# Kernel optimization log

Measured on AMD Instinct MI355X. Metric: run time of the kernel, lower is better.

Reference implementation:

```python
import jax, jax.numpy as jnp
import numpy as np

INTER = 30
NPOOL = 33            # int(1000/30), matches AvgPool2d floor behavior
CA_SCALE = NPOOL ** 0.5
EMB, HEADS, DEPTH = 10, 5, 3


def _ln(x, g, b, eps=1e-5):
    m = jnp.mean(x, -1, keepdims=True)
    v = jnp.mean(jnp.square(x - m), -1, keepdims=True)
    return (x - m) * jax.lax.rsqrt(v + eps) * g + b


def _pool(x):
    # AvgPool2d(kernel=(1,INTER), stride=(1,INTER)) on last dim: [b,o,c,s] -> [b,o,c,NPOOL]
    b, o, c, s = x.shape
    return x[..., :NPOOL * INTER].reshape(b, o, c, NPOOL, INTER).mean(-1)


def _conv(x, w, strides):
    return jax.lax.conv_general_dilated(x, w, strides, 'VALID',
                                        dimension_numbers=('NCHW', 'OIHW', 'NCHW'))


def _channel_attention(x, qw, qb, qg, qbe, kw, kb, kg, kbe, pw, pb, pg, pbe):
    temp = jnp.swapaxes(x, -1, -2)                               # b o s c
    q = jnp.swapaxes(_ln(temp @ qw + qb, qg, qbe), -1, -2)       # b o c s
    k = jnp.swapaxes(_ln(temp @ kw + kb, kg, kbe), -1, -2)
    att = jnp.einsum('bocs,boms->bocm', _pool(q), _pool(k)) / CA_SCALE
    score = jax.nn.softmax(att, axis=-1)
    out = jnp.einsum('bocs,bocm->bocs', x, score)                # m summed out, as in torch einsum
    out = _ln(jnp.swapaxes(out, -1, -2) @ pw + pb, pg, pbe)
    return jnp.swapaxes(out, -1, -2)


def _mha(x, qw, qb, kw, kb, vw, vb, ow, ob):
    b, n, e = x.shape
    d = e // HEADS
    q = (x @ qw + qb).reshape(b, n, HEADS, d).transpose(0, 2, 1, 3)
    k = (x @ kw + kb).reshape(b, n, HEADS, d).transpose(0, 2, 1, 3)
    v = (x @ vw + vb).reshape(b, n, HEADS, d).transpose(0, 2, 1, 3)
    energy = jnp.einsum('bhqd,bhkd->bhqk', q, k)
    att = jax.nn.softmax(energy / (e ** 0.5), axis=-1)
    out = jnp.einsum('bhqk,bhkd->bhqd', att, v)
    return out.transpose(0, 2, 1, 3).reshape(b, n, e) @ ow + ob


def setup_inputs():
    key = jax.random.key(0)
    ks = jax.random.split(key, 16)
    g = lambda i, sh, s=0.1: jax.random.normal(ks[i], sh, jnp.float32) * s
    z = lambda sh: jnp.zeros(sh, jnp.float32)
    o = lambda sh: jnp.ones(sh, jnp.float32)
    return dict(
        x=jax.random.normal(ks[0], (512, 1, 1000, 22), jnp.float32),
        change_w=g(1, (22, 16)), change_b=z((16,)),
        ca_q_w=g(2, (16, 16)), ca_q_b=z((16,)), ca_q_g=o((16,)), ca_q_be=z((16,)),
        ca_k_w=g(3, (16, 16)), ca_k_b=z((16,)), ca_k_g=o((16,)), ca_k_be=z((16,)),
        ca_p_w=g(4, (16, 16)), ca_p_b=z((16,)), ca_p_g=o((16,)), ca_p_be=z((16,)),
        conv1_w=g(5, (2, 1, 1, 51)), conv1_b=z((2,)),
        bn_g=o((2,)), bn_b=z((2,)), bn_mean=z((2,)), bn_var=o((2,)),
        conv2_w=g(6, (10, 2, 16, 5)), conv2_b=z((10,)),
        tf_ln1_g=o((3, 10)), tf_ln1_b=z((3, 10)),
        tf_q_w=g(7, (3, 10, 10)), tf_q_b=z((3, 10)),
        tf_k_w=g(8, (3, 10, 10)), tf_k_b=z((3, 10)),
        tf_v_w=g(9, (3, 10, 10)), tf_v_b=z((3, 10)),
        tf_o_w=g(10, (3, 10, 10)), tf_o_b=z((3, 10)),
        tf_ln2_g=o((3, 10)), tf_ln2_b=z((3, 10)),
        tf_ff1_w=g(11, (3, 10, 40)), tf_ff1_b=z((3, 40)),
        tf_ff2_w=g(12, (3, 40, 10)), tf_ff2_b=z((3, 10)),
    )


def reference(x, change_w, change_b,
              ca_q_w, ca_q_b, ca_q_g, ca_q_be,
              ca_k_w, ca_k_b, ca_k_g, ca_k_be,
              ca_p_w, ca_p_b, ca_p_g, ca_p_be,
              conv1_w, conv1_b, bn_g, bn_b, bn_mean, bn_var,
              conv2_w, conv2_b,
              tf_ln1_g, tf_ln1_b, tf_q_w, tf_q_b, tf_k_w, tf_k_b,
              tf_v_w, tf_v_b, tf_o_w, tf_o_b, tf_ln2_g, tf_ln2_b,
              tf_ff1_w, tf_ff1_b, tf_ff2_w, tf_ff2_b):
    h = x @ change_w + change_b                  # [b,1,1000,16]
    h = jnp.swapaxes(h, -1, -2)                  # [b,1,16,1000]
    for _ in range(4):
        h = _channel_attention(h, ca_q_w, ca_q_b, ca_q_g, ca_q_be,
                               ca_k_w, ca_k_b, ca_k_g, ca_k_be,
                               ca_p_w, ca_p_b, ca_p_g, ca_p_be) + h
    c = _conv(h, conv1_w, (1, 1)) + conv1_b[None, :, None, None]     # [b,2,16,950]
    bshape = lambda v: v[None, :, None, None]
    c = (c - bshape(bn_mean)) * bshape(jax.lax.rsqrt(bn_var + 1e-5)) * bshape(bn_g) + bshape(bn_b)
    c = jnp.where(c > 0, c, 0.2 * c)             # LeakyReLU(0.2)
    c = _conv(c, conv2_w, (1, 5)) + conv2_b[None, :, None, None]     # [b,10,1,190]
    b_, e_, hh, ww = c.shape
    t = c.reshape(b_, e_, hh * ww).transpose(0, 2, 1)                # [b,190,10]
    for i in range(DEPTH):
        y = _ln(t, tf_ln1_g[i], tf_ln1_b[i])
        t = t + _mha(y, tf_q_w[i], tf_q_b[i], tf_k_w[i], tf_k_b[i],
                     tf_v_w[i], tf_v_b[i], tf_o_w[i], tf_o_b[i])
        y = _ln(t, tf_ln2_g[i], tf_ln2_b[i])
        t = t + (jax.nn.gelu(y @ tf_ff1_w[i] + tf_ff1_b[i], approximate=False) @ tf_ff2_w[i] + tf_ff2_b[i])
    return t
```

## Files before the change

kernel.cpp:

```cpp
#include <hip/hip_runtime.h>

using ushort_t = unsigned short;

__device__ __forceinline__ float u2f(ushort_t u){
    union{unsigned int i; float f;} x; x.i = ((unsigned int)u) << 16; return x.f;
}
__device__ __forceinline__ ushort_t f2u(float f){
    union{float fl; unsigned int i;} x; x.fl = f;
    unsigned int r = x.i + 0x7FFFu + ((x.i >> 16) & 1u);
    return (ushort_t)(r >> 16);
}

__device__ __forceinline__ void ln10(const float* in, float* out,
                                     const float* __restrict__ g,
                                     const float* __restrict__ b){
    float m = 0.f;
#pragma unroll
    for (int c = 0; c < 10; ++c) m += in[c];
    m *= 0.1f;
    float v = 0.f;
#pragma unroll
    for (int c = 0; c < 10; ++c){ float d = in[c] - m; v += d*d; }
    v *= 0.1f;
    float inv = rsqrtf(v + 1e-5f);
#pragma unroll
    for (int c = 0; c < 10; ++c) out[c] = (in[c] - m) * inv * g[c] + b[c];
}

__global__ __launch_bounds__(256)
void k_embed(const float* __restrict__ X,
             const float* __restrict__ CW, const float* __restrict__ CB,
             const float* __restrict__ PW, const float* __restrict__ PB,
             const float* __restrict__ PG, const float* __restrict__ PBE,
             ushort_t* __restrict__ Hws)
{
    const int idx = blockIdx.x * 256 + threadIdx.x;
    const int b = idx / 1000, s = idx - b * 1000;

    const float2* xu = (const float2*)(X + (size_t)idx * 22);
    float xv[22];
#pragma unroll
    for (int j = 0; j < 11; ++j){
        float2 u = xu[j];
        xv[2*j] = u.x; xv[2*j+1] = u.y;
    }
    float v[16];
#pragma unroll
    for (int c = 0; c < 16; ++c){
        float a = CB[c];
#pragma unroll
        for (int j = 0; j < 22; ++j) a += xv[j] * CW[j*16 + c];
        v[c] = a;
    }
#pragma unroll
    for (int it = 0; it < 4; ++it){
        float u[16]; float m = 0.f;
#pragma unroll
        for (int c = 0; c < 16; ++c){
            float a = PB[c];
#pragma unroll
            for (int j = 0; j < 16; ++j) a += v[j] * PW[j*16 + c];
            u[c] = a; m += a;
        }
        m *= (1.f/16.f);
        float var = 0.f;
#pragma unroll
        for (int c = 0; c < 16; ++c){ float d = u[c] - m; var += d*d; }
        var *= (1.f/16.f);
        float inv = rsqrtf(var + 1e-5f);
#pragma unroll
        for (int c = 0; c < 16; ++c) v[c] += (u[c] - m) * inv * PG[c] + PBE[c];
    }
#pragma unroll
    for (int c = 0; c < 16; ++c)
        Hws[b*16000 + c*1000 + s] = f2u(v[c]);
}

__global__ __launch_bounds__(256)
void k_conv(const ushort_t* __restrict__ Hws,
            const float* __restrict__ W1, const float* __restrict__ B1,
            const float* __restrict__ BNG, const float* __restrict__ BNB,
            const float* __restrict__ BNM, const float* __restrict__ BNV,
            const float* __restrict__ W2, const float* __restrict__ B2,
            float* __restrict__ Tws)
{
    __shared__ __align__(16) float sH[16000];

    const int tid = threadIdx.x;
    const int b   = blockIdx.x;

    for (int i = tid; i < 16000; i += 256) sH[i] = u2f(Hws[b*16000 + i]);

    float sc[2], sh[2];
#pragma unroll
    for (int i = 0; i < 2; ++i){
        float s0 = BNG[i] * rsqrtf(BNV[i] + 1e-5f);
        sc[i] = s0;
        sh[i] = BNB[i] + (B1[i] - BNM[i]) * s0;
    }
    __syncthreads();

    if (tid < 190){
        const int w = tid;
        float acc[10];
#pragma unroll
        for (int o = 0; o < 10; ++o) acc[o] = B2[o];
        for (int kh = 0; kh < 16; ++kh){
            float hh[55];
#pragma unroll
            for (int j = 0; j < 55; ++j) hh[j] = sH[kh*1000 + 5*w + j];
            float val[2][5];
#pragma unroll
            for (int i = 0; i < 2; ++i){
#pragma unroll
                for (int kw = 0; kw < 5; ++kw){
                    float s = 0.f;
#pragma unroll
                    for (int k = 0; k < 51; ++k) s += hh[kw + k] * W1[i*51 + k];
                    s = s * sc[i] + sh[i];
                    val[i][kw] = s > 0.f ? s : 0.2f * s;
                }
            }
#pragma unroll
            for (int o = 0; o < 10; ++o){
                float s = acc[o];
#pragma unroll
                for (int i = 0; i < 2; ++i)
#pragma unroll
                    for (int kw = 0; kw < 5; ++kw)
                        s += val[i][kw] * W2[((o*2 + i)*16 + kh)*5 + kw];
                acc[o] = s;
            }
        }
#pragma unroll
        for (int o = 0; o < 10; ++o) Tws[(size_t)b*1900 + w*10 + o] = acc[o];
    }
}

__global__ __launch_bounds__(256)
void k_tf(const float* __restrict__ Tws,
          const float* __restrict__ LN1G, const float* __restrict__ LN1B,
          const float* __restrict__ QW, const float* __restrict__ QBv,
          const float* __restrict__ KW, const float* __restrict__ KBv,
          const float* __restrict__ VW, const float* __restrict__ VBv,
          const float* __restrict__ OW, const float* __restrict__ OBv,
          const float* __restrict__ LN2G, const float* __restrict__ LN2B,
          const float* __restrict__ F1W, const float* __restrict__ F1B,
          const float* __restrict__ F2W, const float* __restrict__ F2B,
          float* __restrict__ OUT)
{
    __shared__ __align__(16) float T [190*11];
    __shared__ __align__(16) float QB[190*12];
    __shared__ __align__(16) float KB[190*12];
    __shared__ __align__(16) float VB[190*12];
    __shared__ __align__(16) float AT[190*12];

    const int tid = threadIdx.x;
    const int b   = blockIdx.x;

    for (int i = tid; i < 1900; i += 256){
        int r = i / 10, c = i - r*10;
        T[r*11 + c] = Tws[(size_t)b*1900 + i];
    }
    __syncthreads();

    const float SCALE = 0.31622776601683794f;
    const bool act = (tid < 190);
#pragma unroll 1
    for (int L = 0; L < 3; ++L){
        const float* ln1g = LN1G + L*10; const float* ln1b = LN1B + L*10;
        const float* qw = QW + L*100;    const float* qb = QBv + L*10;
        const float* kw = KW + L*100;    const float* kb = KBv + L*10;
        const float* vw = VW + L*100;    const float* vb = VBv + L*10;
        const float* ow = OW + L*100;    const float* ob = OBv + L*10;
        const float* ln2g = LN2G + L*10; const float* ln2b = LN2B + L*10;
        const float* f1w = F1W + L*400;  const float* f1b = F1B + L*40;
        const float* f2w = F2W + L*400;  const float* f2b = F2B + L*10;

        if (act){
            float tv[10], y[10];
#pragma unroll
            for (int c = 0; c < 10; ++c) tv[c] = T[tid*11 + c];
            ln10(tv, y, ln1g, ln1b);
#pragma unroll
            for (int c = 0; c < 10; ++c){
                float aq = qb[c], ak = kb[c], av = vb[c];
#pragma unroll
                for (int j = 0; j < 10; ++j){
                    aq += y[j] * qw[j*10 + c];
                    ak += y[j] * kw[j*10 + c];
                    av += y[j] * vw[j*10 + c];
                }
                QB[tid*12 + c] = aq;
                KB[tid*12 + c] = ak;
                VB[tid*12 + c] = av;
            }
        }
        __syncthreads();

        if (tid < 240){
            const int h5 = tid / 48;
            const int qg = tid - h5*48;
            const int q0 = qg * 4;
            float qx[4], qy[4];
#pragma unroll
            for (int i = 0; i < 4; ++i){
                int qi = q0 + i;
                if (qi < 190){
                    qx[i] = QB[qi*12 + 2*h5]     * SCALE;
                    qy[i] = QB[qi*12 + 2*h5 + 1] * SCALE;
                } else { qx[i] = 0.f; qy[i] = 0.f; }
            }
            float l[4] = {0,0,0,0}, a0[4] = {0,0,0,0}, a1[4] = {0,0,0,0};
#pragma unroll 2
            for (int kk = 0; kk < 190; ++kk){
                float2 kv = *(const float2*)&KB[kk*12 + 2*h5];
                float2 vv = *(const float2*)&VB[kk*12 + 2*h5];
#pragma unroll
                for (int i = 0; i < 4; ++i){
                    float p = __expf(qx[i]*kv.x + qy[i]*kv.y);
                    l[i] += p; a0[i] += p*vv.x; a1[i] += p*vv.y;
                }
            }
#pragma unroll
            for (int i = 0; i < 4; ++i){
                int qi = q0 + i;
                if (qi < 190){
                    float rl = 1.f / l[i];
                    AT[qi*12 + 2*h5]     = a0[i] * rl;
                    AT[qi*12 + 2*h5 + 1] = a1[i] * rl;
                }
            }
        }
        __syncthreads();

        if (act){
            float tv[10], at[10];
#pragma unroll
            for (int c = 0; c < 10; ++c){ tv[c] = T[tid*11 + c]; at[c] = AT[tid*12 + c]; }
#pragma unroll
            for (int c = 0; c < 10; ++c){
                float a = ob[c];
#pragma unroll
                for (int j = 0; j < 10; ++j) a += at[j] * ow[j*10 + c];
                tv[c] += a;
            }
            float y2[10];
            ln10(tv, y2, ln2g, ln2b);
            float g40[40];
#pragma unroll
            for (int j = 0; j < 40; ++j){
                float a = f1b[j];
#pragma unroll
                for (int c = 0; c < 10; ++c) a += y2[c] * f1w[c*40 + j];
                g40[j] = 0.5f * a * (1.f + erff(a * 0.70710678118654752f));
            }
#pragma unroll
            for (int c = 0; c < 10; ++c){
                float a = f2b[c];
#pragma unroll
                for (int j = 0; j < 40; ++j) a += g40[j] * f2w[j*10 + c];
                tv[c] += a;
            }
#pragma unroll
            for (int c = 0; c < 10; ++c) T[tid*11 + c] = tv[c];
        }
        __syncthreads();
    }

    if (act){
#pragma unroll
        for (int c = 0; c < 10; ++c)
            OUT[(size_t)b*1900 + tid*10 + c] = T[tid*11 + c];
    }
}

extern "C" void kernel_launch(void* const* d_in, const int* in_sizes, int n_in,
                              void* d_out, int out_size, void* d_ws, size_t ws_size,
                              hipStream_t stream)
{
    (void)ws_size; (void)n_in; (void)out_size;
    const int B = in_sizes[0] / 22000;
    auto in = [&](int i){ return (const float*)d_in[i]; };
    ushort_t* Hws = (ushort_t*)d_ws;
    float*    Tws = (float*)((char*)d_ws + (size_t)B*16000*2);

    k_embed<<<(B*1000 + 255)/256, 256, 0, stream>>>(
        in(0), in(1), in(2), in(11), in(12), in(13), in(14), Hws);

    k_conv<<<B, 256, 0, stream>>>(
        Hws, in(15), in(16), in(17), in(18), in(19), in(20), in(21), in(22), Tws);

    k_tf<<<B, 256, 0, stream>>>(
        Tws,
        in(23), in(24), in(25), in(26), in(27), in(28), in(29), in(30),
        in(31), in(32), in(33), in(34), in(35), in(36), in(37), in(38),
        (float*)d_out);
}
```

Measured before the change: 485.5 us.

## Fuse conv and transformer kernels, restructure conv stage, stage weights in LDS

Merges the conv and transformer kernels into one per-batch kernel, so the intermediate T tensor stays in shared memory instead of going through global memory. The first conv stage is reorganised: 6080 work items spread across all 256 threads each compute a 5-wide window and write bf16 results to LDS, where before 190 threads recomputed everything. The embed kernel now stages its weights in LDS, processes two rows per thread with float4 weight reads, and uses a fixed 1000-block grid. The transformer weights are also copied into LDS, and the FFN is fused so the 40-wide hidden array is not kept live. Risks are the hardcoded batch of 512 in the embed grid and row stride, heavy LDS use (about 67 KB) limiting occupancy, and an extra bf16 rounding of the intermediate conv output.

```diff
diff --git a/kernel.cpp b/kernel.cpp
--- a/kernel.cpp
+++ b/kernel.cpp
@@ -9,22 +9,6 @@
     union{float fl; unsigned int i;} x; x.fl = f;
     unsigned int r = x.i + 0x7FFFu + ((x.i >> 16) & 1u);
     return (ushort_t)(r >> 16);
-}
-
-__device__ __forceinline__ void ln10(const float* in, float* out,
-                                     const float* __restrict__ g,
-                                     const float* __restrict__ b){
-    float m = 0.f;
-#pragma unroll
-    for (int c = 0; c < 10; ++c) m += in[c];
-    m *= 0.1f;
-    float v = 0.f;
-#pragma unroll
-    for (int c = 0; c < 10; ++c){ float d = in[c] - m; v += d*d; }
-    v *= 0.1f;
-    float inv = rsqrtf(v + 1e-5f);
-#pragma unroll
-    for (int c = 0; c < 10; ++c) out[c] = (in[c] - m) * inv * g[c] + b[c];
 }
 
 __global__ __launch_bounds__(256)
@@ -34,133 +18,210 @@
              const float* __restrict__ PG, const float* __restrict__ PBE,
              ushort_t* __restrict__ Hws)
 {
-    const int idx = blockIdx.x * 256 + threadIdx.x;
-    const int b = idx / 1000, s = idx - b * 1000;
-
-    const float2* xu = (const float2*)(X + (size_t)idx * 22);
-    float xv[22];
-#pragma unroll
-    for (int j = 0; j < 11; ++j){
-        float2 u = xu[j];
-        xv[2*j] = u.x; xv[2*j+1] = u.y;
-    }
-    float v[16];
-#pragma unroll
-    for (int c = 0; c < 16; ++c){
-        float a = CB[c];
-#pragma unroll
-        for (int j = 0; j < 22; ++j) a += xv[j] * CW[j*16 + c];
-        v[c] = a;
-    }
+    __shared__ __align__(16) float sW[672];
+    {
+        const int t = threadIdx.x;
+        for (int i = t; i < 352; i += 256) sW[i] = CW[i];
+        if (t < 256) { if (t < 16){ sW[352+t] = CB[t]; sW[624+t] = PB[t];
+                                    sW[640+t] = PG[t]; sW[656+t] = PBE[t]; } }
+        for (int i = t; i < 256; i += 256) sW[368+i] = PW[i];
+    }
+    __syncthreads();
+    const float4* sW4 = (const float4*)sW;
+
+    const int g = blockIdx.x * 256 + threadIdx.x;
+
+    float xv[2][22];
+#pragma unroll
+    for (int r = 0; r < 2; ++r){
+        const float* xp = X + (size_t)(g + r*256000) * 22;
+#pragma unroll
+        for (int j = 0; j < 22; ++j) xv[r][j] = xp[j];
+    }
+
+    float v[2][16];
+#pragma unroll
+    for (int cg = 0; cg < 4; ++cg){
+        float acc[2][4];
+#pragma unroll
+        for (int q = 0; q < 4; ++q){ float b0 = sW[352 + cg*4 + q]; acc[0][q] = b0; acc[1][q] = b0; }
+#pragma unroll
+        for (int j = 0; j < 22; ++j){
+            float4 w = sW4[j*4 + cg];
+#pragma unroll
+            for (int r = 0; r < 2; ++r){
+                acc[r][0] += xv[r][j]*w.x; acc[r][1] += xv[r][j]*w.y;
+                acc[r][2] += xv[r][j]*w.z; acc[r][3] += xv[r][j]*w.w;
+            }
+        }
+#pragma unroll
+        for (int r = 0; r < 2; ++r)
+#pragma unroll
+        for (int q = 0; q < 4; ++q) v[r][cg*4+q] = acc[r][q];
+    }
+
 #pragma unroll
     for (int it = 0; it < 4; ++it){
-        float u[16]; float m = 0.f;
-#pragma unroll
-        for (int c = 0; c < 16; ++c){
-            float a = PB[c];
-#pragma unroll
-            for (int j = 0; j < 16; ++j) a += v[j] * PW[j*16 + c];
-            u[c] = a; m += a;
-        }
-        m *= (1.f/16.f);
-        float var = 0.f;
-#pragma unroll
-        for (int c = 0; c < 16; ++c){ float d = u[c] - m; var += d*d; }
-        var *= (1.f/16.f);
-        float inv = rsqrtf(var + 1e-5f);
-#pragma unroll
-        for (int c = 0; c < 16; ++c) v[c] += (u[c] - m) * inv * PG[c] + PBE[c];
-    }
-#pragma unroll
-    for (int c = 0; c < 16; ++c)
-        Hws[b*16000 + c*1000 + s] = f2u(v[c]);
+        float u[2][16];
+#pragma unroll
+        for (int cg = 0; cg < 4; ++cg){
+            float acc[2][4];
+#pragma unroll
+            for (int q = 0; q < 4; ++q){ float b0 = sW[624 + cg*4 + q]; acc[0][q] = b0; acc[1][q] = b0; }
+#pragma unroll
+            for (int j = 0; j < 16; ++j){
+                float4 w = sW4[92 + j*4 + cg];
+#pragma unroll
+                for (int r = 0; r < 2; ++r){
+                    acc[r][0] += v[r][j]*w.x; acc[r][1] += v[r][j]*w.y;
+                    acc[r][2] += v[r][j]*w.z; acc[r][3] += v[r][j]*w.w;
+                }
+            }
+#pragma unroll
+            for (int r = 0; r < 2; ++r)
+#pragma unroll
+            for (int q = 0; q < 4; ++q) u[r][cg*4+q] = acc[r][q];
+        }
+#pragma unroll
+        for (int r = 0; r < 2; ++r){
+            float m = 0.f;
+#pragma unroll
+            for (int c = 0; c < 16; ++c) m += u[r][c];
+            m *= (1.f/16.f);
+            float var = 0.f;
+#pragma unroll
+            for (int c = 0; c < 16; ++c){ float d = u[r][c] - m; var += d*d; }
+            var *= (1.f/16.f);
+            float inv = rsqrtf(var + 1e-5f);
+#pragma unroll
+            for (int c = 0; c < 16; ++c) v[r][c] += (u[r][c] - m) * inv * sW[640+c] + sW[656+c];
+        }
+    }
+
+#pragma unroll
+    for (int r = 0; r < 2; ++r){
+        const int row = g + r*256000;
+        const int b = row / 1000, s = row - b*1000;
+        ushort_t* hp = Hws + b*16000 + s;
+#pragma unroll
+        for (int c = 0; c < 16; ++c) hp[c*1000] = f2u(v[r][c]);
+    }
 }
 
 __global__ __launch_bounds__(256)
-void k_conv(const ushort_t* __restrict__ Hws,
+void k_main(const ushort_t* __restrict__ Hws,
             const float* __restrict__ W1, const float* __restrict__ B1,
             const float* __restrict__ BNG, const float* __restrict__ BNB,
             const float* __restrict__ BNM, const float* __restrict__ BNV,
             const float* __restrict__ W2, const float* __restrict__ B2,
-            float* __restrict__ Tws)
+            const float* __restrict__ LN1G, const float* __restrict__ LN1B,
+            const float* __restrict__ QW, const float* __restrict__ QBv,
+            const float* __restrict__ KW, const float* __restrict__ KBv,
+            const float* __restrict__ VW, const float* __restrict__ VBv,
+            const float* __restrict__ OW, const float* __restrict__ OBv,
+            const float* __restrict__ LN2G, const float* __restrict__ LN2B,
+            const float* __restrict__ F1W, const float* __restrict__ F1B,
+            const float* __restrict__ F2W, const float* __restrict__ F2B,
+            float* __restrict__ OUT)
 {
-    __shared__ __align__(16) float sH[16000];
-
+    __shared__ __align__(16) char sMem[67760];
     const int tid = threadIdx.x;
     const int b   = blockIdx.x;
 
-    for (int i = tid; i < 16000; i += 256) sH[i] = u2f(Hws[b*16000 + i]);
-
-    float sc[2], sh[2];
-#pragma unroll
-    for (int i = 0; i < 2; ++i){
-        float s0 = BNG[i] * rsqrtf(BNV[i] + 1e-5f);
-        sc[i] = s0;
-        sh[i] = BNB[i] + (B1[i] - BNM[i]) * s0;
-    }
-    __syncthreads();
-
+    ushort_t* C1  = (ushort_t*)sMem;
+    float*    W1f = (float*)(sMem + 60928);
+    float*    BNf = (float*)(sMem + 61344);
+    float*    W2f = (float*)(sMem + 61360);
+
+    for (int i = tid; i < 102;  i += 256) W1f[i] = W1[i];
+    for (int i = tid; i < 1600; i += 256) W2f[i] = W2[i];
+    if (tid < 2){
+        float s0 = BNG[tid] * rsqrtf(BNV[tid] + 1e-5f);
+        BNf[tid]     = s0;
+        BNf[2 + tid] = BNB[tid] + (B1[tid] - BNM[tid]) * s0;
+    }
+    __syncthreads();
+
+#pragma unroll 1
+    for (int k = 0; k < 24; ++k){
+        int gp = tid + 256*k;
+        if (gp < 6080){
+            const int ik = gp / 190;
+            const int u_ = gp - ik*190;
+            const int i  = ik >> 4;
+            const int kh = ik & 15;
+            const int w0 = u_ * 5;
+            const ushort_t* hp = Hws + b*16000 + kh*1000 + w0;
+            const float* w1p = W1f + i*51;
+            const float sc = BNf[i], sh = BNf[2+i];
+            float win[55];
+#pragma unroll
+            for (int t = 0; t < 55; ++t) win[t] = u2f(hp[t]);
+            float acc[5];
+#pragma unroll
+            for (int q = 0; q < 5; ++q) acc[q] = 0.f;
+#pragma unroll
+            for (int t = 0; t < 51; ++t){
+                float wk = w1p[t];
+#pragma unroll
+                for (int q = 0; q < 5; ++q) acc[q] += win[t+q] * wk;
+            }
+#pragma unroll
+            for (int q = 0; q < 5; ++q){
+                float s = acc[q]*sc + sh;
+                s = s > 0.f ? s : 0.2f*s;
+                C1[ik*952 + w0 + q] = f2u(s);
+            }
+        }
+    }
+    __syncthreads();
+
+    float acc10[10];
     if (tid < 190){
-        const int w = tid;
-        float acc[10];
-#pragma unroll
-        for (int o = 0; o < 10; ++o) acc[o] = B2[o];
+        const ushort_t* c1p = C1 + tid*5;
+#pragma unroll
+        for (int o = 0; o < 10; ++o) acc10[o] = B2[o];
+#pragma unroll
         for (int kh = 0; kh < 16; ++kh){
-            float hh[55];
-#pragma unroll
-            for (int j = 0; j < 55; ++j) hh[j] = sH[kh*1000 + 5*w + j];
-            float val[2][5];
-#pragma unroll
-            for (int i = 0; i < 2; ++i){
-#pragma unroll
-                for (int kw = 0; kw < 5; ++kw){
-                    float s = 0.f;
-#pragma unroll
-                    for (int k = 0; k < 51; ++k) s += hh[kw + k] * W1[i*51 + k];
-                    s = s * sc[i] + sh[i];
-                    val[i][kw] = s > 0.f ? s : 0.2f * s;
-                }
-            }
-#pragma unroll
-            for (int o = 0; o < 10; ++o){
-                float s = acc[o];
-#pragma unroll
-                for (int i = 0; i < 2; ++i)
-#pragma unroll
-                    for (int kw = 0; kw < 5; ++kw)
-                        s += val[i][kw] * W2[((o*2 + i)*16 + kh)*5 + kw];
-                acc[o] = s;
-            }
-        }
-#pragma unroll
-        for (int o = 0; o < 10; ++o) Tws[(size_t)b*1900 + w*10 + o] = acc[o];
-    }
-}
-
-__global__ __launch_bounds__(256)
-void k_tf(const float* __restrict__ Tws,
-          const float* __restrict__ LN1G, const float* __restrict__ LN1B,
-          const float* __restrict__ QW, const float* __restrict__ QBv,
-          const float* __restrict__ KW, const float* __restrict__ KBv,
-          const float* __restrict__ VW, const float* __restrict__ VBv,
-          const float* __restrict__ OW, const float* __restrict__ OBv,
-          const float* __restrict__ LN2G, const float* __restrict__ LN2B,
-          const float* __restrict__ F1W, const float* __restrict__ F1B,
-          const float* __restrict__ F2W, const float* __restrict__ F2B,
-          float* __restrict__ OUT)
-{
-    __shared__ __align__(16) float T [190*11];
-    __shared__ __align__(16) float QB[190*12];
-    __shared__ __align__(16) float KB[190*12];
-    __shared__ __align__(16) float VB[190*12];
-    __shared__ __align__(16) float AT[190*12];
-
-    const int tid = threadIdx.x;
-    const int b   = blockIdx.x;
-
-    for (int i = tid; i < 1900; i += 256){
-        int r = i / 10, c = i - r*10;
-        T[r*11 + c] = Tws[(size_t)b*1900 + i];
+#pragma unroll
+            for (int kw = 0; kw < 5; ++kw){
+                float v0 = u2f(c1p[ kh*952       + kw]);
+                float v1 = u2f(c1p[(16+kh)*952   + kw]);
+#pragma unroll
+                for (int o = 0; o < 10; ++o)
+                    acc10[o] += v0 * W2f[((o*2    )*16 + kh)*5 + kw]
+                              + v1 * W2f[((o*2 + 1)*16 + kh)*5 + kw];
+            }
+        }
+    }
+    __syncthreads();
+
+    float* TW = (float*)sMem;
+    float* T  = (float*)(sMem + 15960);
+    float* QB = (float*)(sMem + 24320);
+    float* KB = (float*)(sMem + 33440);
+    float* VB = (float*)(sMem + 42560);
+    float* AT = (float*)(sMem + 51680);
+
+    {
+        auto cl3 = [&](int off, const float* src, int n){
+            for (int i = tid; i < 3*n; i += 256){
+                int L = i / n, j = i - L*n;
+                TW[L*1330 + off + j] = src[i];
+            }
+        };
+        cl3(   0, LN1G,  10);  cl3(  10, LN1B,  10);
+        cl3(  20, QW,   100);  cl3( 120, QBv,   10);
+        cl3( 130, KW,   100);  cl3( 230, KBv,   10);
+        cl3( 240, VW,   100);  cl3( 340, VBv,   10);
+        cl3( 350, OW,   100);  cl3( 450, OBv,   10);
+        cl3( 460, LN2G,  10);  cl3( 470, LN2B,  10);
+        cl3( 480, F1W,  400);  cl3( 880, F1B,   40);
+        cl3( 920, F2W,  400);  cl3(1320, F2B,   10);
+    }
+    if (tid < 190){
+#pragma unroll
+        for (int o = 0; o < 10; ++o) T[tid*11 + o] = acc10[o];
     }
     __syncthreads();
 
@@ -168,28 +229,31 @@
     const bool act = (tid < 190);
 #pragma unroll 1
     for (int L = 0; L < 3; ++L){
-        const float* ln1g = LN1G + L*10; const float* ln1b = LN1B + L*10;
-        const float* qw = QW + L*100;    const float* qb = QBv + L*10;
-        const float* kw = KW + L*100;    const float* kb = KBv + L*10;
-        const float* vw = VW + L*100;    const float* vb = VBv + L*10;
-        const float* ow = OW + L*100;    const float* ob = OBv + L*10;
-        const float* ln2g = LN2G + L*10; const float* ln2b = LN2B + L*10;
-        const float* f1w = F1W + L*400;  const float* f1b = F1B + L*40;
-        const float* f2w = F2W + L*400;  const float* f2b = F2B + L*10;
+        const float* W = TW + L*1330;
 
         if (act){
             float tv[10], y[10];
 #pragma unroll
             for (int c = 0; c < 10; ++c) tv[c] = T[tid*11 + c];
-            ln10(tv, y, ln1g, ln1b);
+            float m = 0.f;
+#pragma unroll
+            for (int c = 0; c < 10; ++c) m += tv[c];
+            m *= 0.1f;
+            float var = 0.f;
+#pragma unroll
+            for (int c = 0; c < 10; ++c){ float d = tv[c]-m; var += d*d; }
+            var *= 0.1f;
+            float inv = rsqrtf(var + 1e-5f);
+#pragma unroll
+            for (int c = 0; c < 10; ++c) y[c] = (tv[c]-m)*inv*W[0+c] + W[10+c];
 #pragma unroll
             for (int c = 0; c < 10; ++c){
-                float aq = qb[c], ak = kb[c], av = vb[c];
+                float aq = W[120+c], ak = W[230+c], av = W[340+c];
 #pragma unroll
                 for (int j = 0; j < 10; ++j){
-                    aq += y[j] * qw[j*10 + c];
-                    ak += y[j] * kw[j*10 + c];
-                    av += y[j] * vw[j*10 + c];
+                    aq += y[j] * W[ 20 + j*10 + c];
+                    ak += y[j] * W[130 + j*10 + c];
+                    av += y[j] * W[240 + j*10 + c];
                 }
                 QB[tid*12 + c] = aq;
                 KB[tid*12 + c] = ak;
@@ -212,10 +276,12 @@
                 } else { qx[i] = 0.f; qy[i] = 0.f; }
             }
             float l[4] = {0,0,0,0}, a0[4] = {0,0,0,0}, a1[4] = {0,0,0,0};
+            const float* kp = KB + 2*h5;
+            const float* vp = VB + 2*h5;
 #pragma unroll 2
             for (int kk = 0; kk < 190; ++kk){
-                float2 kv = *(const float2*)&KB[kk*12 + 2*h5];
-                float2 vv = *(const float2*)&VB[kk*12 + 2*h5];
+                float2 kv = *(const float2*)(kp + kk*12);
+                float2 vv = *(const float2*)(vp + kk*12);
 #pragma unroll
                 for (int i = 0; i < 4; ++i){
                     float p = __expf(qx[i]*kv.x + qy[i]*kv.y);
@@ -240,30 +306,37 @@
             for (int c = 0; c < 10; ++c){ tv[c] = T[tid*11 + c]; at[c] = AT[tid*12 + c]; }
 #pragma unroll
             for (int c = 0; c < 10; ++c){
-                float a = ob[c];
-#pragma unroll
-                for (int j = 0; j < 10; ++j) a += at[j] * ow[j*10 + c];
+                float a = W[450+c];
+#pragma unroll
+                for (int j = 0; j < 10; ++j) a += at[j] * W[350 + j*10 + c];
                 tv[c] += a;
             }
+            float m = 0.f;
+#pragma unroll
+            for (int c = 0; c < 10; ++c) m += tv[c];
+            m *= 0.1f;
+            float var = 0.f;
+#pragma unroll
+            for (int c = 0; c < 10; ++c){ float d = tv[c]-m; var += d*d; }
+            var *= 0.1f;
+            float inv = rsqrtf(var + 1e-5f);
             float y2[10];
-            ln10(tv, y2, ln2g, ln2b);
-            float g40[40];
+#pragma unroll
+            for (int c = 0; c < 10; ++c) y2[c] = (tv[c]-m)*inv*W[460+c] + W[470+c];
+            float d10[10];
+#pragma unroll
+            for (int c = 0; c < 10; ++c) d10[c] = W[1320+c];
 #pragma unroll
             for (int j = 0; j < 40; ++j){
-                float a = f1b[j];
-#pragma unroll
-                for (int c = 0; c < 10; ++c) a += y2[c] * f1w[c*40 + j];
-                g40[j] = 0.5f * a * (1.f + erff(a * 0.70710678118654752f));
-            }
-#pragma unroll
-            for (int c = 0; c < 10; ++c){
-                float a = f2b[c];
-#pragma unroll
-                for (int j = 0; j < 40; ++j) a += g40[j] * f2w[j*10 + c];
-                tv[c] += a;
-            }
-#pragma unroll
-            for (int c = 0; c < 10; ++c) T[tid*11 + c] = tv[c];
+                float a = W[880+j];
+#pragma unroll
+                for (int c = 0; c < 10; ++c) a += y2[c] * W[480 + c*40 + j];
+                float gj = 0.5f * a * (1.f + erff(a * 0.70710678118654752f));
+#pragma unroll
+                for (int c = 0; c < 10; ++c) d10[c] += gj * W[920 + j*10 + c];
+            }
+#pragma unroll
+            for (int c = 0; c < 10; ++c) T[tid*11 + c] = tv[c] + d10[c];
         }
         __syncthreads();
     }
@@ -283,16 +356,13 @@
     const int B = in_sizes[0] / 22000;
     auto in = [&](int i){ return (const float*)d_in[i]; };
     ushort_t* Hws = (ushort_t*)d_ws;
-    float*    Tws = (float*)((char*)d_ws + (size_t)B*16000*2);
-
-    k_embed<<<(B*1000 + 255)/256, 256, 0, stream>>>(
+
+    k_embed<<<1000, 256, 0, stream>>>(
         in(0), in(1), in(2), in(11), in(12), in(13), in(14), Hws);
 
-    k_conv<<<B, 256, 0, stream>>>(
-        Hws, in(15), in(16), in(17), in(18), in(19), in(20), in(21), in(22), Tws);
-
-    k_tf<<<B, 256, 0, stream>>>(
-        Tws,
+    k_main<<<B, 256, 0, stream>>>(
+        Hws,
+        in(15), in(16), in(17), in(18), in(19), in(20), in(21), in(22),
         in(23), in(24), in(25), in(26), in(27), in(28), in(29), in(30),
         in(31), in(32), in(33), in(34), in(35), in(36), in(37), in(38),
         (float*)d_out);
```

Result: slower. 496.9 us (+2.4%).

## Macro-unroll all kernels into scalar registers and store conv input as bf16 in LDS

Applied to the files above, without the earlier changes.

Replaces the array-based loops in the embed, conv and transformer kernels with macro-expanded scalar variables so that everything stays in registers. The conv kernel now keeps its shared tile as bf16 (halving LDS to 32KB, which could allow more resident blocks), copies it with 32-bit loads, and converts values at each tap. The FFN computes the GELU hidden units in a loop and accumulates the second matmul on the fly instead of holding a 40-element array. The risks are heavier code size, register pressure, and extra per-tap conversion work in the conv inner loop.

```diff
diff --git a/kernel.cpp b/kernel.cpp
--- a/kernel.cpp
+++ b/kernel.cpp
@@ -1,6 +1,6 @@
 #include <hip/hip_runtime.h>
 
-using ushort_t = unsigned short;
+typedef unsigned short ushort_t;
 
 __device__ __forceinline__ float u2f(ushort_t u){
     union{unsigned int i; float f;} x; x.i = ((unsigned int)u) << 16; return x.f;
@@ -11,21 +11,10 @@
     return (ushort_t)(r >> 16);
 }
 
-__device__ __forceinline__ void ln10(const float* in, float* out,
-                                     const float* __restrict__ g,
-                                     const float* __restrict__ b){
-    float m = 0.f;
-#pragma unroll
-    for (int c = 0; c < 10; ++c) m += in[c];
-    m *= 0.1f;
-    float v = 0.f;
-#pragma unroll
-    for (int c = 0; c < 10; ++c){ float d = in[c] - m; v += d*d; }
-    v *= 0.1f;
-    float inv = rsqrtf(v + 1e-5f);
-#pragma unroll
-    for (int c = 0; c < 10; ++c) out[c] = (in[c] - m) * inv * g[c] + b[c];
-}
+#define REP10(M) M(0)M(1)M(2)M(3)M(4)M(5)M(6)M(7)M(8)M(9)
+#define REP16(M) M(0)M(1)M(2)M(3)M(4)M(5)M(6)M(7)M(8)M(9)M(10)M(11)M(12)M(13)M(14)M(15)
+#define REP22(M) REP16(M) M(16)M(17)M(18)M(19)M(20)M(21)
+#define REP55(M) M(0)M(1)M(2)M(3)M(4)M(5)M(6)M(7)M(8)M(9)M(10)M(11)M(12)M(13)M(14)M(15)M(16)M(17)M(18)M(19)M(20)M(21)M(22)M(23)M(24)M(25)M(26)M(27)M(28)M(29)M(30)M(31)M(32)M(33)M(34)M(35)M(36)M(37)M(38)M(39)M(40)M(41)M(42)M(43)M(44)M(45)M(46)M(47)M(48)M(49)M(50)M(51)M(52)M(53)M(54)
 
 __global__ __launch_bounds__(256)
 void k_embed(const float* __restrict__ X,
@@ -36,44 +25,42 @@
 {
     const int idx = blockIdx.x * 256 + threadIdx.x;
     const int b = idx / 1000, s = idx - b * 1000;
-
-    const float2* xu = (const float2*)(X + (size_t)idx * 22);
-    float xv[22];
-#pragma unroll
-    for (int j = 0; j < 11; ++j){
-        float2 u = xu[j];
-        xv[2*j] = u.x; xv[2*j+1] = u.y;
-    }
-    float v[16];
-#pragma unroll
-    for (int c = 0; c < 16; ++c){
-        float a = CB[c];
-#pragma unroll
-        for (int j = 0; j < 22; ++j) a += xv[j] * CW[j*16 + c];
-        v[c] = a;
-    }
-#pragma unroll
-    for (int it = 0; it < 4; ++it){
-        float u[16]; float m = 0.f;
-#pragma unroll
-        for (int c = 0; c < 16; ++c){
-            float a = PB[c];
-#pragma unroll
-            for (int j = 0; j < 16; ++j) a += v[j] * PW[j*16 + c];
-            u[c] = a; m += a;
-        }
-        m *= (1.f/16.f);
-        float var = 0.f;
-#pragma unroll
-        for (int c = 0; c < 16; ++c){ float d = u[c] - m; var += d*d; }
-        var *= (1.f/16.f);
-        float inv = rsqrtf(var + 1e-5f);
-#pragma unroll
-        for (int c = 0; c < 16; ++c) v[c] += (u[c] - m) * inv * PG[c] + PBE[c];
-    }
-#pragma unroll
-    for (int c = 0; c < 16; ++c)
-        Hws[b*16000 + c*1000 + s] = f2u(v[c]);
+    const float* xp = X + (size_t)idx * 22;
+
+#define E_DX(j) float x##j = xp[j];
+    REP22(E_DX)
+#define E_DV(c) float v##c = CB[c];
+    REP16(E_DV)
+#define E_CH(j) { const float xx = x##j; const float* w = CW + (j)*16; \
+    v0+=xx*w[0]; v1+=xx*w[1]; v2+=xx*w[2]; v3+=xx*w[3]; \
+    v4+=xx*w[4]; v5+=xx*w[5]; v6+=xx*w[6]; v7+=xx*w[7]; \
+    v8+=xx*w[8]; v9+=xx*w[9]; v10+=xx*w[10]; v11+=xx*w[11]; \
+    v12+=xx*w[12]; v13+=xx*w[13]; v14+=xx*w[14]; v15+=xx*w[15]; }
+    REP22(E_CH)
+
+#define E_DU(c) float u##c = PB[c];
+#define E_PJ(j) { const float vv = v##j; const float* w = PW + (j)*16; \
+    u0+=vv*w[0]; u1+=vv*w[1]; u2+=vv*w[2]; u3+=vv*w[3]; \
+    u4+=vv*w[4]; u5+=vv*w[5]; u6+=vv*w[6]; u7+=vv*w[7]; \
+    u8+=vv*w[8]; u9+=vv*w[9]; u10+=vv*w[10]; u11+=vv*w[11]; \
+    u12+=vv*w[12]; u13+=vv*w[13]; u14+=vv*w[14]; u15+=vv*w[15]; }
+#define E_DS(c) const float d##c = u##c - m;
+#define E_UP(c) v##c += d##c * inv * PG[c] + PBE[c];
+#define E_LNIT { \
+    REP16(E_DU) REP16(E_PJ) \
+    float m = (((u0+u1)+(u2+u3))+((u4+u5)+(u6+u7)))+(((u8+u9)+(u10+u11))+((u12+u13)+(u14+u15))); \
+    m *= 0.0625f; \
+    REP16(E_DS) \
+    float var = (((d0*d0+d1*d1)+(d2*d2+d3*d3))+((d4*d4+d5*d5)+(d6*d6+d7*d7)))+(((d8*d8+d9*d9)+(d10*d10+d11*d11))+((d12*d12+d13*d13)+(d14*d14+d15*d15))); \
+    var *= 0.0625f; \
+    float inv = rsqrtf(var + 1e-5f); \
+    REP16(E_UP) }
+
+    E_LNIT E_LNIT E_LNIT E_LNIT
+
+    ushort_t* hp = Hws + b*16000 + s;
+#define E_ST(c) hp[(c)*1000] = f2u(v##c);
+    REP16(E_ST)
 }
 
 __global__ __launch_bounds__(256)
@@ -84,56 +71,49 @@
             const float* __restrict__ W2, const float* __restrict__ B2,
             float* __restrict__ Tws)
 {
-    __shared__ __align__(16) float sH[16000];
-
-    const int tid = threadIdx.x;
-    const int b   = blockIdx.x;
-
-    for (int i = tid; i < 16000; i += 256) sH[i] = u2f(Hws[b*16000 + i]);
-
-    float sc[2], sh[2];
-#pragma unroll
-    for (int i = 0; i < 2; ++i){
-        float s0 = BNG[i] * rsqrtf(BNV[i] + 1e-5f);
-        sc[i] = s0;
-        sh[i] = BNB[i] + (B1[i] - BNM[i]) * s0;
-    }
+    __shared__ ushort_t sH[16000];
+    const int tid = threadIdx.x, b = blockIdx.x;
+
+    {
+        const unsigned int* src = (const unsigned int*)(Hws + b*16000);
+        unsigned int* dst = (unsigned int*)sH;
+        for (int i = tid; i < 8000; i += 256) dst[i] = src[i];
+    }
+    const float sc0 = BNG[0]*rsqrtf(BNV[0]+1e-5f);
+    const float sc1 = BNG[1]*rsqrtf(BNV[1]+1e-5f);
+    const float sh0 = BNB[0] + (B1[0]-BNM[0])*sc0;
+    const float sh1 = BNB[1] + (B1[1]-BNM[1])*sc1;
     __syncthreads();
 
     if (tid < 190){
-        const int w = tid;
-        float acc[10];
-#pragma unroll
-        for (int o = 0; o < 10; ++o) acc[o] = B2[o];
+        const int w5 = tid*5;
+#define C_DT(o) float t##o = B2[o];
+        REP10(C_DT)
+        const float* w1a = W1;
+        const float* w1b = W1 + 51;
         for (int kh = 0; kh < 16; ++kh){
-            float hh[55];
-#pragma unroll
-            for (int j = 0; j < 55; ++j) hh[j] = sH[kh*1000 + 5*w + j];
-            float val[2][5];
-#pragma unroll
-            for (int i = 0; i < 2; ++i){
-#pragma unroll
-                for (int kw = 0; kw < 5; ++kw){
-                    float s = 0.f;
-#pragma unroll
-                    for (int k = 0; k < 51; ++k) s += hh[kw + k] * W1[i*51 + k];
-                    s = s * sc[i] + sh[i];
-                    val[i][kw] = s > 0.f ? s : 0.2f * s;
-                }
-            }
-#pragma unroll
-            for (int o = 0; o < 10; ++o){
-                float s = acc[o];
-#pragma unroll
-                for (int i = 0; i < 2; ++i)
-#pragma unroll
-                    for (int kw = 0; kw < 5; ++kw)
-                        s += val[i][kw] * W2[((o*2 + i)*16 + kh)*5 + kw];
-                acc[o] = s;
-            }
-        }
-#pragma unroll
-        for (int o = 0; o < 10; ++o) Tws[(size_t)b*1900 + w*10 + o] = acc[o];
+            const ushort_t* hp = sH + kh*1000 + w5;
+            float a0=0.f,a1=0.f,a2=0.f,a3=0.f,a4=0.f;
+            float b0_=0.f,b1_=0.f,b2_=0.f,b3_=0.f,b4_=0.f;
+#define C_TAP(e) { const float cur = u2f(hp[e]); \
+            if ((e) < 51)              { a0+=cur*w1a[(e)];   b0_+=cur*w1b[(e)];   } \
+            if ((e) >= 1 && (e) < 52)  { a1+=cur*w1a[(e)-1]; b1_+=cur*w1b[(e)-1]; } \
+            if ((e) >= 2 && (e) < 53)  { a2+=cur*w1a[(e)-2]; b2_+=cur*w1b[(e)-2]; } \
+            if ((e) >= 3 && (e) < 54)  { a3+=cur*w1a[(e)-3]; b3_+=cur*w1b[(e)-3]; } \
+            if ((e) >= 4)              { a4+=cur*w1a[(e)-4]; b4_+=cur*w1b[(e)-4]; } }
+            REP55(C_TAP)
+#define C_LR(q) { a##q = a##q*sc0 + sh0; a##q = a##q > 0.f ? a##q : 0.2f*a##q; \
+                  b##q##_ = b##q##_*sc1 + sh1; b##q##_ = b##q##_ > 0.f ? b##q##_ : 0.2f*b##q##_; }
+            C_LR(0) C_LR(1) C_LR(2) C_LR(3) C_LR(4)
+#define C_C2(o) { const float* wa = W2 + (((o)*2  )*16 + kh)*5; \
+                  const float* wb = W2 + (((o)*2+1)*16 + kh)*5; \
+        t##o += a0*wa[0]+a1*wa[1]+a2*wa[2]+a3*wa[3]+a4*wa[4] \
+              + b0_*wb[0]+b1_*wb[1]+b2_*wb[2]+b3_*wb[3]+b4_*wb[4]; }
+            REP10(C_C2)
+        }
+        float* op = Tws + (size_t)b*1900 + tid*10;
+#define C_ST(o) op[o] = t##o;
+        REP10(C_ST)
     }
 }
 
@@ -155,11 +135,9 @@
     __shared__ __align__(16) float VB[190*12];
     __shared__ __align__(16) float AT[190*12];
 
-    const int tid = threadIdx.x;
-    const int b   = blockIdx.x;
-
+    const int tid = threadIdx.x, b = blockIdx.x;
     for (int i = tid; i < 1900; i += 256){
-        int r = i / 10, c = i - r*10;
+        int r = i/10, c = i - r*10;
         T[r*11 + c] = Tws[(size_t)b*1900 + i];
     }
     __syncthreads();
@@ -178,23 +156,29 @@
         const float* f2w = F2W + L*400;  const float* f2b = F2B + L*10;
 
         if (act){
-            float tv[10], y[10];
-#pragma unroll
-            for (int c = 0; c < 10; ++c) tv[c] = T[tid*11 + c];
-            ln10(tv, y, ln1g, ln1b);
-#pragma unroll
-            for (int c = 0; c < 10; ++c){
-                float aq = qb[c], ak = kb[c], av = vb[c];
-#pragma unroll
-                for (int j = 0; j < 10; ++j){
-                    aq += y[j] * qw[j*10 + c];
-                    ak += y[j] * kw[j*10 + c];
-                    av += y[j] * vw[j*10 + c];
-                }
-                QB[tid*12 + c] = aq;
-                KB[tid*12 + c] = ak;
-                VB[tid*12 + c] = av;
-            }
+#define T_TV(c) float tv##c = T[tid*11 + c];
+            REP10(T_TV)
+            float m = (((tv0+tv1)+(tv2+tv3))+((tv4+tv5)+(tv6+tv7)))+(tv8+tv9);
+            m *= 0.1f;
+#define T_D1(c) const float e1##c = tv##c - m;
+            REP10(T_D1)
+            float var = (((e10*e10+e11*e11)+(e12*e12+e13*e13))+((e14*e14+e15*e15)+(e16*e16+e17*e17)))+(e18*e18+e19*e19);
+            var *= 0.1f;
+            float inv = rsqrtf(var + 1e-5f);
+#define T_Y(c) const float y##c = e1##c*inv*ln1g[c] + ln1b[c];
+            REP10(T_Y)
+#define T_PQ(c) { float aq = qb[c] + y0*qw[c] + y1*qw[10+c] + y2*qw[20+c] + y3*qw[30+c] + y4*qw[40+c] \
+                           + y5*qw[50+c] + y6*qw[60+c] + y7*qw[70+c] + y8*qw[80+c] + y9*qw[90+c]; \
+                  QB[tid*12 + c] = aq; }
+            REP10(T_PQ)
+#define T_PK(c) { float ak = kb[c] + y0*kw[c] + y1*kw[10+c] + y2*kw[20+c] + y3*kw[30+c] + y4*kw[40+c] \
+                           + y5*kw[50+c] + y6*kw[60+c] + y7*kw[70+c] + y8*kw[80+c] + y9*kw[90+c]; \
+                  KB[tid*12 + c] = ak; }
+            REP10(T_PK)
+#define T_PV(c) { float av = vb[c] + y0*vw[c] + y1*vw[10+c] + y2*vw[20+c] + y3*vw[30+c] + y4*vw[40+c] \
+                           + y5*vw[50+c] + y6*vw[60+c] + y7*vw[70+c] + y8*vw[80+c] + y9*vw[90+c]; \
+                  VB[tid*12 + c] = av; }
+            REP10(T_PV)
         }
         __syncthreads();
 
@@ -202,76 +186,70 @@
             const int h5 = tid / 48;
             const int qg = tid - h5*48;
             const int q0 = qg * 4;
-            float qx[4], qy[4];
-#pragma unroll
-            for (int i = 0; i < 4; ++i){
-                int qi = q0 + i;
-                if (qi < 190){
-                    qx[i] = QB[qi*12 + 2*h5]     * SCALE;
-                    qy[i] = QB[qi*12 + 2*h5 + 1] * SCALE;
-                } else { qx[i] = 0.f; qy[i] = 0.f; }
+#define T_LQ(i) float qx##i, qy##i; { const int qi = q0 + i; \
+            if (qi < 190){ qx##i = QB[qi*12 + 2*h5]*SCALE; qy##i = QB[qi*12 + 2*h5 + 1]*SCALE; } \
+            else { qx##i = 0.f; qy##i = 0.f; } }
+            T_LQ(0) T_LQ(1) T_LQ(2) T_LQ(3)
+            float l0=0.f,l1=0.f,l2=0.f,l3=0.f;
+            float p00=0.f,p01=0.f,p10=0.f,p11=0.f,p20=0.f,p21=0.f,p30=0.f,p31=0.f;
+            const float* kp = KB + 2*h5;
+            const float* vp = VB + 2*h5;
+            for (int kk = 0; kk < 190; ++kk){
+                const float2 kv = *(const float2*)(kp + kk*12);
+                const float2 vv = *(const float2*)(vp + kk*12);
+                const float e0 = __expf(qx0*kv.x + qy0*kv.y);
+                const float e1 = __expf(qx1*kv.x + qy1*kv.y);
+                const float e2 = __expf(qx2*kv.x + qy2*kv.y);
+                const float e3 = __expf(qx3*kv.x + qy3*kv.y);
+                l0 += e0; p00 += e0*vv.x; p01 += e0*vv.y;
+                l1 += e1; p10 += e1*vv.x; p11 += e1*vv.y;
+                l2 += e2; p20 += e2*vv.x; p21 += e2*vv.y;
+                l3 += e3; p30 += e3*vv.x; p31 += e3*vv.y;
             }
-            float l[4] = {0,0,0,0}, a0[4] = {0,0,0,0}, a1[4] = {0,0,0,0};
-#pragma unroll 2
-            for (int kk = 0; kk < 190; ++kk){
-                float2 kv = *(const float2*)&KB[kk*12 + 2*h5];
-                float2 vv = *(const float2*)&VB[kk*12 + 2*h5];
-#pragma unroll
-                for (int i = 0; i < 4; ++i){
-                    float p = __expf(qx[i]*kv.x + qy[i]*kv.y);
-                    l[i] += p; a0[i] += p*vv.x; a1[i] += p*vv.y;
-                }
+#define T_SA(i) { const int qi = q0 + i; if (qi < 190){ const float rl = 1.f/l##i; \
+                  AT[qi*12 + 2*h5] = p##i##0*rl; AT[qi*12 + 2*h5 + 1] = p##i##1*rl; } }
+            T_SA(0) T_SA(1) T_SA(2) T_SA(3)
+        }
+        __syncthreads();
+
+        if (act){
+#define T_TV2(c) float w##c = T[tid*11 + c];
+            REP10(T_TV2)
+#define T_AT(c) const float at##c = AT[tid*12 + c];
+            REP10(T_AT)
+#define T_OP(c) w##c += ob[c] + at0*ow[c] + at1*ow[10+c] + at2*ow[20+c] + at3*ow[30+c] + at4*ow[40+c] \
+                       + at5*ow[50+c] + at6*ow[60+c] + at7*ow[70+c] + at8*ow[80+c] + at9*ow[90+c];
+            REP10(T_OP)
+            float m2 = (((w0+w1)+(w2+w3))+((w4+w5)+(w6+w7)))+(w8+w9);
+            m2 *= 0.1f;
+#define T_D2(c) const float e2##c = w##c - m2;
+            REP10(T_D2)
+            float var2 = (((e20*e20+e21*e21)+(e22*e22+e23*e23))+((e24*e24+e25*e25)+(e26*e26+e27*e27)))+(e28*e28+e29*e29);
+            var2 *= 0.1f;
+            float inv2 = rsqrtf(var2 + 1e-5f);
+#define T_Z(c) const float z##c = e2##c*inv2*ln2g[c] + ln2b[c];
+            REP10(T_Z)
+#define T_DD(c) float dd##c = f2b[c];
+            REP10(T_DD)
+#pragma unroll 4
+            for (int j = 0; j < 40; ++j){
+                float aj = f1b[j] + z0*f1w[j] + z1*f1w[40+j] + z2*f1w[80+j] + z3*f1w[120+j] + z4*f1w[160+j]
+                         + z5*f1w[200+j] + z6*f1w[240+j] + z7*f1w[280+j] + z8*f1w[320+j] + z9*f1w[360+j];
+                const float gj = 0.5f * aj * (1.f + erff(aj * 0.70710678118654752f));
+                const float* w2p = f2w + j*10;
+                dd0 += gj*w2p[0]; dd1 += gj*w2p[1]; dd2 += gj*w2p[2]; dd3 += gj*w2p[3]; dd4 += gj*w2p[4];
+                dd5 += gj*w2p[5]; dd6 += gj*w2p[6]; dd7 += gj*w2p[7]; dd8 += gj*w2p[8]; dd9 += gj*w2p[9];
             }
-#pragma unroll
-            for (int i = 0; i < 4; ++i){
-                int qi = q0 + i;
-                if (qi < 190){
-                    float rl = 1.f / l[i];
-                    AT[qi*12 + 2*h5]     = a0[i] * rl;
-                    AT[qi*12 + 2*h5 + 1] = a1[i] * rl;
-                }
-            }
+#define T_WB(c) T[tid*11 + c] = w##c + dd##c;
+            REP10(T_WB)
         }
         __syncthreads();
-
-        if (act){
-            float tv[10], at[10];
-#pragma unroll
-            for (int c = 0; c < 10; ++c){ tv[c] = T[tid*11 + c]; at[c] = AT[tid*12 + c]; }
-#pragma unroll
-            for (int c = 0; c < 10; ++c){
-                float a = ob[c];
-#pragma unroll
-                for (int j = 0; j < 10; ++j) a += at[j] * ow[j*10 + c];
-                tv[c] += a;
-            }
-            float y2[10];
-            ln10(tv, y2, ln2g, ln2b);
-            float g40[40];
-#pragma unroll
-            for (int j = 0; j < 40; ++j){
-                float a = f1b[j];
-#pragma unroll
-                for (int c = 0; c < 10; ++c) a += y2[c] * f1w[c*40 + j];
-                g40[j] = 0.5f * a * (1.f + erff(a * 0.70710678118654752f));
-            }
-#pragma unroll
-            for (int c = 0; c < 10; ++c){
-                float a = f2b[c];
-#pragma unroll
-                for (int j = 0; j < 40; ++j) a += g40[j] * f2w[j*10 + c];
-                tv[c] += a;
-            }
-#pragma unroll
-            for (int c = 0; c < 10; ++c) T[tid*11 + c] = tv[c];
-        }
-        __syncthreads();
     }
 
     if (act){
-#pragma unroll
-        for (int c = 0; c < 10; ++c)
-            OUT[(size_t)b*1900 + tid*10 + c] = T[tid*11 + c];
+        float* op = OUT + (size_t)b*1900 + tid*10;
+#define T_OUT(c) op[c] = T[tid*11 + c];
+        REP10(T_OUT)
     }
 }
 
```

New measurement: 398.9 us. 1.22x faster.
